# Optimization experiments

Hardware: AMD Instinct MI355X
Metric: run time of the kernel (lower is better)

The kernel has to match this reference:

```python
import jax, jax.numpy as jnp
import numpy as np

N, E, IN, HID, OUT = 100000, 1600000, 128, 128, 64


def _gcn(x, w, b, src, dst, norm, n):
    # PyG GCNConv: linear transform, then normalized scatter-add aggregation
    h = x @ w                                  # [N, F_out]
    msg = h[src] * norm[:, None]               # gather + scale, [E', F_out]
    agg = jax.ops.segment_sum(msg, dst, num_segments=n)
    return agg + b


def setup_inputs() -> dict:
    key = jax.random.key(0)
    ks = jax.random.split(key, 10)
    s = 0.05
    return {
        "X": jax.random.normal(ks[0], (N, IN), jnp.float32),
        "edge_index": jax.random.randint(ks[1], (2, E), 0, N, jnp.int64),
        "unused": 0,
        "gw1": jax.random.normal(ks[2], (IN, HID), jnp.float32) * s,
        "gb1": jnp.zeros((HID,), jnp.float32),
        "lw1": jax.random.normal(ks[3], (IN, HID), jnp.float32) * s,
        "lb1": jnp.zeros((HID,), jnp.float32),
        "gw2": jax.random.normal(ks[4], (HID, HID), jnp.float32) * s,
        "gb2": jnp.zeros((HID,), jnp.float32),
        "lw2": jax.random.normal(ks[5], (HID, HID), jnp.float32) * s,
        "lb2": jnp.zeros((HID,), jnp.float32),
        "gw3": jax.random.normal(ks[6], (HID, HID), jnp.float32) * s,
        "gb3": jnp.zeros((HID,), jnp.float32),
        "lw3": jax.random.normal(ks[7], (HID, HID), jnp.float32) * s,
        "lb3": jnp.zeros((HID,), jnp.float32),
        "fcw": jax.random.normal(ks[8], (HID, OUT), jnp.float32) * s,
        "fcb": jnp.zeros((OUT,), jnp.float32),
    }


def reference(X, edge_index, unused, gw1, gb1, lw1, lb1, gw2, gb2, lw2, lb2,
              gw3, gb3, lw3, lb3, fcw, fcb):
    n = X.shape[0]
    loop = jnp.arange(n)
    src = jnp.concatenate([edge_index[0], loop])   # self-loops appended
    dst = jnp.concatenate([edge_index[1], loop])
    deg = jax.ops.segment_sum(jnp.ones_like(dst, dtype=X.dtype), dst, num_segments=n)
    dis = jnp.where(deg > 0, jax.lax.rsqrt(jnp.maximum(deg, 1e-12)), 0.0)
    norm = dis[src] * dis[dst]                     # D^-1/2 (A+I) D^-1/2 weights

    lrelu = lambda v: jax.nn.leaky_relu(v, negative_slope=0.01)
    h = lrelu(_gcn(X, gw1, gb1, src, dst, norm, n) + X @ lw1 + lb1)
    h = lrelu(_gcn(h, gw2, gb2, src, dst, norm, n) + h @ lw2 + lb2)
    h = lrelu(_gcn(h, gw3, gb3, src, dst, norm, n) + h @ lw3 + lb3)
    y = h @ fcw + fcb
    return (h, y)
```

## Files before the change

### kernel.cpp

```cpp
#include <hip/hip_runtime.h>
#include <cstdint>
#include <cstddef>


typedef __attribute__((ext_vector_type(4))) float f32x4;
typedef __attribute__((ext_vector_type(8))) short bf16x8;
typedef unsigned short u16;

#define G_CHUNKS 256

__device__ __forceinline__ float bf2f(unsigned int u) {
  union { unsigned int i; float f; } v;
  v.i = u << 16;
  return v.f;
}
__device__ __forceinline__ u16 f2bf(float f) {
  union { float f; unsigned int i; } v;
  v.f = f;
  unsigned int i = v.i;
  return (u16)((i + 0x7FFFu + ((i >> 16) & 1u)) >> 16);
}


__global__ __launch_bounds__(256) void k_hist(const int* __restrict__ ei,
                                              int* __restrict__ ghist,
                                              int E, int B, int chunk) {
  __shared__ int h[512];
  for (int t = threadIdx.x; t < B; t += 256) h[t] = 0;
  __syncthreads();
  const int g = blockIdx.x;
  const int beg = g * chunk;
  const int end = min(beg + chunk, E);
  for (int e = beg + threadIdx.x; e < end; e += 256)
    atomicAdd(&h[ei[E + e] >> 8], 1);
  __syncthreads();
  for (int t = threadIdx.x; t < B; t += 256) ghist[(size_t)t * G_CHUNKS + g] = h[t];
}

__global__ __launch_bounds__(256) void k_hscan(int* __restrict__ ghist,
                                               int* __restrict__ btot) {
  __shared__ int sm[256];
  int* p = ghist + (size_t)blockIdx.x * G_CHUNKS;
  const int t = threadIdx.x;
  int v = p[t];
  sm[t] = v;
  __syncthreads();
  for (int off = 1; off < 256; off <<= 1) {
    int u = (t >= off) ? sm[t - off] : 0;
    __syncthreads();
    sm[t] += u;
    __syncthreads();
  }
  p[t] = sm[t] - v;
  if (t == 255) btot[blockIdx.x] = sm[255];
}

__global__ __launch_bounds__(512) void k_bscan(const int* __restrict__ btot,
                                               int* __restrict__ boff, int B,
                                               int* __restrict__ rowptr, int n,
                                               int E, int tot) {
  __shared__ int sm[512];
  const int t = threadIdx.x;
  int v = (t < B) ? btot[t] : 0;
  sm[t] = v;
  __syncthreads();
  for (int off = 1; off < 512; off <<= 1) {
    int u = (t >= off) ? sm[t - off] : 0;
    __syncthreads();
    sm[t] += u;
    __syncthreads();
  }
  if (t < B) boff[t] = sm[t] - v;
  if (t == 0) {
    boff[B] = E;
    rowptr[n] = tot;
  }
}

__global__ __launch_bounds__(256) void k_scatter(const int* __restrict__ ei,
                                                 const int* __restrict__ ghist,
                                                 const int* __restrict__ boff,
                                                 unsigned int* __restrict__ ebuf,
                                                 int E, int B, int chunk) {
  __shared__ int off[512];
  const int g = blockIdx.x;
  for (int t = threadIdx.x; t < B; t += 256)
    off[t] = boff[t] + ghist[(size_t)t * G_CHUNKS + g];
  __syncthreads();
  const int beg = g * chunk;
  const int end = min(beg + chunk, E);
  for (int e = beg + threadIdx.x; e < end; e += 256) {
    int s = ei[e];
    int d = ei[E + e];
    int pos = atomicAdd(&off[d >> 8], 1);
    ebuf[pos] = ((unsigned int)s << 8) | (unsigned int)(d & 255);
  }
}

__global__ __launch_bounds__(256) void k_cfill(const unsigned int* __restrict__ ebuf,
                                               const int* __restrict__ boff,
                                               int* __restrict__ rowptr,
                                               int* __restrict__ col,
                                               float* __restrict__ dis, int n) {
  __shared__ int cnt[256];
  __shared__ int fl[256];
  const int b = blockIdx.x;
  const int t = threadIdx.x;
  const int beg = boff[b];
  const int end = boff[b + 1];
  const int node0 = b << 8;
  const int nn = min(256, n - node0);
  cnt[t] = 0;
  __syncthreads();
  for (int e = beg + t; e < end; e += 256)
    atomicAdd(&cnt[ebuf[e] & 255u], 1);
  __syncthreads();
  int v = cnt[t];
  __shared__ int sm[256];
  sm[t] = v;
  __syncthreads();
  for (int off = 1; off < 256; off <<= 1) {
    int u = (t >= off) ? sm[t - off] : 0;
    __syncthreads();
    sm[t] += u;
    __syncthreads();
  }
  if (t < nn) {
    int excl = sm[t] - v;
    int rbase = beg + node0 + t + excl;
    int i = node0 + t;
    rowptr[i] = rbase;
    col[rbase] = i;
    fl[t] = rbase + 1;
    dis[i] = rsqrtf((float)(v + 1));
  }
  __syncthreads();
  for (int e = beg + t; e < end; e += 256) {
    unsigned int pk = ebuf[e];
    int pos = atomicAdd(&fl[pk & 255u], 1);
    col[pos] = (int)(pk >> 8);
  }
}


__global__ __launch_bounds__(256) void k_cvt(const float* __restrict__ src,
                                             const float* __restrict__ dis,
                                             u16* __restrict__ dstb,
                                             u16* __restrict__ dsts, int total8) {
  int i = blockIdx.x * 256 + threadIdx.x;
  if (i >= total8) return;
  size_t b = (size_t)i * 8;
  float ds = dis[i >> 4];
  float4 a0 = *(const float4*)(src + b);
  float4 a1 = *(const float4*)(src + b + 4);
  u16 ob[8] = {f2bf(a0.x), f2bf(a0.y), f2bf(a0.z), f2bf(a0.w),
               f2bf(a1.x), f2bf(a1.y), f2bf(a1.z), f2bf(a1.w)};
  u16 os[8] = {f2bf(a0.x * ds), f2bf(a0.y * ds), f2bf(a0.z * ds), f2bf(a0.w * ds),
               f2bf(a1.x * ds), f2bf(a1.y * ds), f2bf(a1.z * ds), f2bf(a1.w * ds)};
  *(ulonglong2*)(dstb + b) = *(ulonglong2*)ob;
  *(ulonglong2*)(dsts + b) = *(ulonglong2*)os;
}

__global__ __launch_bounds__(128) void k_prep(const float* __restrict__ w0,
                                              const float* __restrict__ w1,
                                              const float* __restrict__ w2,
                                              const float* __restrict__ w3,
                                              const float* __restrict__ w4,
                                              const float* __restrict__ w5,
                                              const float* __restrict__ g1,
                                              const float* __restrict__ l1,
                                              const float* __restrict__ g2,
                                              const float* __restrict__ l2,
                                              const float* __restrict__ g3,
                                              const float* __restrict__ l3,
                                              const float* __restrict__ fcw,
                                              u16* __restrict__ wt,
                                              float* __restrict__ bias,
                                              u16* __restrict__ fcT) {
  int bx = blockIdx.x;
  if (bx < 768) {
    int z = bx >> 7, nr = bx & 127, k = threadIdx.x;
    const float* Ws[6] = {w0, w1, w2, w3, w4, w5};
    wt[(size_t)z * 16384 + nr * 128 + k] = f2bf(Ws[z][k * 128 + nr]);
  } else if (bx < 771) {
    int t = (bx - 768) * 128 + threadIdx.x;
    if (t < 384) {
      const float* gs[3] = {g1, g2, g3};
      const float* ls[3] = {l1, l2, l3};
      bias[t] = gs[t >> 7][t & 127] + ls[t >> 7][t & 127];
    }
  } else {
    int nr = bx - 771;
    int k = threadIdx.x;
    fcT[nr * 128 + k] = f2bf(fcw[k * 64 + nr]);
  }
}

__global__ __launch_bounds__(256, 4) void k_spmv_bf(const int* __restrict__ rowptr,
                                                    const int* __restrict__ col,
                                                    const float* __restrict__ dis,
                                                    const u16* __restrict__ Xs,
                                                    u16* __restrict__ SXb, int n) {
  const int wave = threadIdx.x >> 6;
  const int lane = threadIdx.x & 63;
  const int i = blockIdx.x * 4 + wave;
  if (i >= n) return;
  int j = rowptr[i];
  const int end = rowptr[i + 1];
  float ax = 0.f, ay = 0.f;

#define ROWQ(c) (*(const unsigned int*)(Xs + (size_t)(c) * 128 + lane * 2))
#define ACC(q)  do { unsigned int _q = (q); \
                     ax += bf2f(_q & 0xffffu); ay += bf2f(_q >> 16); } while (0)

  for (; (j & 3) && j < end; ++j) ACC(ROWQ(col[j]));
  for (; j + 7 < end; j += 8) {
    int4 c0 = *(const int4*)(col + j);
    int4 c1 = *(const int4*)(col + j + 4);
    unsigned int q0 = ROWQ(c0.x), q1 = ROWQ(c0.y), q2 = ROWQ(c0.z), q3 = ROWQ(c0.w);
    unsigned int q4 = ROWQ(c1.x), q5 = ROWQ(c1.y), q6 = ROWQ(c1.z), q7 = ROWQ(c1.w);
    ACC(q0); ACC(q1); ACC(q2); ACC(q3);
    ACC(q4); ACC(q5); ACC(q6); ACC(q7);
  }
  if (j + 3 < end) {
    int4 c0 = *(const int4*)(col + j);
    unsigned int q0 = ROWQ(c0.x), q1 = ROWQ(c0.y), q2 = ROWQ(c0.z), q3 = ROWQ(c0.w);
    ACC(q0); ACC(q1); ACC(q2); ACC(q3);
    j += 4;
  }
  for (; j < end; ++j) ACC(ROWQ(col[j]));
#undef ROWQ
#undef ACC

  float di = dis[i];
  ax *= di;
  ay *= di;
  unsigned int o = (unsigned int)f2bf(ax) | ((unsigned int)f2bf(ay) << 16);
  *(unsigned int*)(SXb + (size_t)i * 128 + lane * 2) = o;
}

__global__ __launch_bounds__(256, 6) void k_mfma(const u16* __restrict__ A0,
                                                 const u16* __restrict__ A1,
                                                 const u16* __restrict__ W0T,
                                                 const u16* __restrict__ W1T,
                                                 const float* __restrict__ bias,
                                                 const float* __restrict__ dis,
                                                 u16* __restrict__ outb,
                                                 u16* __restrict__ outs,
                                                 float* __restrict__ outf, int M) {
  const int lane = threadIdx.x & 63;
  const int wv = threadIdx.x >> 6;
  const int row0 = blockIdx.x * 128 + wv * 32;
  const int c0off = blockIdx.y * 64;
  const int r = lane & 15;
  const int kg = lane >> 4;

  f32x4 acc[2][4];
#pragma unroll
  for (int a = 0; a < 2; ++a)
#pragma unroll
    for (int j = 0; j < 4; ++j) acc[a][j] = (f32x4){0.f, 0.f, 0.f, 0.f};

  const int ra0 = min(row0 + r, M - 1);
  const int ra1 = min(row0 + 16 + r, M - 1);

#pragma unroll
  for (int p = 0; p < 2; ++p) {
    const u16* A = p ? A1 : A0;
    const u16* WT = p ? W1T : W0T;
#pragma unroll
    for (int kk = 0; kk < 4; ++kk) {
      const int k0 = kk * 32 + kg * 8;
      bf16x8 a0 = *(const bf16x8*)(A + (size_t)ra0 * 128 + k0);
      bf16x8 a1 = *(const bf16x8*)(A + (size_t)ra1 * 128 + k0);
#pragma unroll
      for (int j = 0; j < 4; ++j) {
        bf16x8 b = *(const bf16x8*)(WT + (size_t)(c0off + j * 16 + r) * 128 + k0);
        acc[0][j] = __builtin_amdgcn_mfma_f32_16x16x32_bf16(a0, b, acc[0][j], 0, 0, 0);
        acc[1][j] = __builtin_amdgcn_mfma_f32_16x16x32_bf16(a1, b, acc[1][j], 0, 0, 0);
      }
    }
  }

#pragma unroll
  for (int rf = 0; rf < 2; ++rf)
#pragma unroll
    for (int e = 0; e < 4; ++e) {
      const int row = row0 + rf * 16 + kg * 4 + e;
      if (row >= M) continue;
      const float ds = outs ? dis[row] : 0.f;
#pragma unroll
      for (int j = 0; j < 4; ++j) {
        const int c = c0off + j * 16 + r;
        float v = acc[rf][j][e] + bias[c];
        v = (v > 0.f) ? v : 0.01f * v;
        if (outf) outf[(size_t)row * 128 + c] = v;
        if (outb) outb[(size_t)row * 128 + c] = f2bf(v);
        if (outs) outs[(size_t)row * 128 + c] = f2bf(v * ds);
      }
    }
}

__global__ __launch_bounds__(256) void k_fc_mfma(const u16* __restrict__ hb3,
                                                 const u16* __restrict__ fcT,
                                                 const float* __restrict__ fcb,
                                                 float* __restrict__ y, int M) {
  const int lane = threadIdx.x & 63;
  const int wv = threadIdx.x >> 6;
  const int row0 = blockIdx.x * 128 + wv * 32;
  const int r = lane & 15;
  const int kg = lane >> 4;

  f32x4 acc[2][4];
#pragma unroll
  for (int a = 0; a < 2; ++a)
#pragma unroll
    for (int j = 0; j < 4; ++j) acc[a][j] = (f32x4){0.f, 0.f, 0.f, 0.f};

  const int ra0 = min(row0 + r, M - 1);
  const int ra1 = min(row0 + 16 + r, M - 1);

#pragma unroll
  for (int kk = 0; kk < 4; ++kk) {
    const int k0 = kk * 32 + kg * 8;
    bf16x8 a0 = *(const bf16x8*)(hb3 + (size_t)ra0 * 128 + k0);
    bf16x8 a1 = *(const bf16x8*)(hb3 + (size_t)ra1 * 128 + k0);
#pragma unroll
    for (int j = 0; j < 4; ++j) {
      bf16x8 b = *(const bf16x8*)(fcT + (size_t)(j * 16 + r) * 128 + k0);
      acc[0][j] = __builtin_amdgcn_mfma_f32_16x16x32_bf16(a0, b, acc[0][j], 0, 0, 0);
      acc[1][j] = __builtin_amdgcn_mfma_f32_16x16x32_bf16(a1, b, acc[1][j], 0, 0, 0);
    }
  }

#pragma unroll
  for (int rf = 0; rf < 2; ++rf)
#pragma unroll
    for (int e = 0; e < 4; ++e) {
      const int row = row0 + rf * 16 + kg * 4 + e;
      if (row >= M) continue;
#pragma unroll
      for (int j = 0; j < 4; ++j) {
        const int c = j * 16 + r;
        y[(size_t)row * 64 + c] = acc[rf][j][e] + fcb[c];
      }
    }
}


extern "C" void kernel_launch(void* const* d_in, const int* in_sizes, int n_in,
                              void* d_out, int out_size, void* d_ws, size_t ws_size,
                              hipStream_t stream) {
  const float* X  = (const float*)d_in[0];
  const int* ei   = (const int*)d_in[1];
  const float* gw1 = (const float*)d_in[3];
  const float* gb1 = (const float*)d_in[4];
  const float* lw1 = (const float*)d_in[5];
  const float* lb1 = (const float*)d_in[6];
  const float* gw2 = (const float*)d_in[7];
  const float* gb2 = (const float*)d_in[8];
  const float* lw2 = (const float*)d_in[9];
  const float* lb2 = (const float*)d_in[10];
  const float* gw3 = (const float*)d_in[11];
  const float* gb3 = (const float*)d_in[12];
  const float* lw3 = (const float*)d_in[13];
  const float* lb3 = (const float*)d_in[14];
  const float* fcw = (const float*)d_in[15];
  const float* fcb = (const float*)d_in[16];

  const int n = in_sizes[0] / 128;
  const int E = in_sizes[1] / 2;
  const int tot = E + n;
  const int B = (n + 255) >> 8;
  const int chunk = (E + G_CHUNKS - 1) / G_CHUNKS;

  char* ws = (char*)d_ws;
  size_t off = 0;
  auto alloc = [&](size_t bytes) -> void* {
    void* p = ws + off;
    off = (off + bytes + 255) & ~(size_t)255;
    return p;
  };
  int* ghist   = (int*)alloc((size_t)B * G_CHUNKS * 4);
  int* btot    = (int*)alloc(512 * 4);
  int* boff    = (int*)alloc((size_t)(B + 1) * 4);
  int* rowptr  = (int*)alloc((size_t)(n + 1) * 4);
  float* dis   = (float*)alloc((size_t)n * 4);
  int* col     = (int*)alloc((size_t)tot * 4);
  unsigned int* ebuf = (unsigned int*)alloc((size_t)E * 4);
  u16* Xb      = (u16*)alloc((size_t)n * 128 * 2);
  u16* Xs      = (u16*)alloc((size_t)n * 128 * 2);
  u16* SXb     = (u16*)alloc((size_t)n * 128 * 2);
  u16* WT      = (u16*)alloc((size_t)6 * 16384 * 2);
  u16* fcT     = (u16*)alloc((size_t)64 * 128 * 2);
  float* bias  = (float*)alloc(384 * 4);

  float* outh = (float*)d_out;
  float* outy = outh + (size_t)n * 128;
  u16* hb = (u16*)outy;

  const int gM = (n + 127) / 128;
  const int gW = (n + 3) / 4;
  const int g8 = (n * 128 / 8 + 255) / 256;

  k_hist<<<G_CHUNKS, 256, 0, stream>>>(ei, ghist, E, B, chunk);
  k_hscan<<<B, 256, 0, stream>>>(ghist, btot);
  k_bscan<<<1, 512, 0, stream>>>(btot, boff, B, rowptr, n, E, tot);
  k_scatter<<<G_CHUNKS, 256, 0, stream>>>(ei, ghist, boff, ebuf, E, B, chunk);
  k_cfill<<<B, 256, 0, stream>>>(ebuf, boff, rowptr, col, dis, n);

  k_cvt<<<g8, 256, 0, stream>>>(X, dis, Xb, Xs, n * 128 / 8);
  k_prep<<<835, 128, 0, stream>>>(gw1, lw1, gw2, lw2, gw3, lw3,
                                  gb1, lb1, gb2, lb2, gb3, lb3, fcw,
                                  WT, bias, fcT);

  k_spmv_bf<<<gW, 256, 0, stream>>>(rowptr, col, dis, Xs, SXb, n);
  k_mfma<<<dim3(gM, 2), 256, 0, stream>>>(SXb, Xb, WT, WT + 16384, bias, dis,
                                          hb, Xs, nullptr, n);
  k_spmv_bf<<<gW, 256, 0, stream>>>(rowptr, col, dis, Xs, SXb, n);
  k_mfma<<<dim3(gM, 2), 256, 0, stream>>>(SXb, hb, WT + 2 * 16384, WT + 3 * 16384,
                                          bias + 128, dis, Xb, Xs, nullptr, n);
  k_spmv_bf<<<gW, 256, 0, stream>>>(rowptr, col, dis, Xs, SXb, n);
  k_mfma<<<dim3(gM, 2), 256, 0, stream>>>(SXb, Xb, WT + 4 * 16384, WT + 5 * 16384,
                                          bias + 256, dis, hb, nullptr, outh, n);
  k_fc_mfma<<<gM, 256, 0, stream>>>(hb, fcT, fcb, outy, n);
}
```

Measured before the change: 470.8 us.

## Use half-wave per row in SpMV and narrow MFMA column tiles

The SpMV kernel now gives each 128-wide row to a 32-lane half-wave, and each lane loads 8-byte bf16 chunks instead of 4-byte ones. Each block therefore covers 8 rows and more gathers are in flight per wave. The fused GEMM kernel now computes 32 output columns per block instead of 64 across a 4-wide grid, with occupancy hints raised to 8. The GEMM split doubles how often the A operand is read, in exchange for fewer registers and more blocks.

```diff
diff --git a/kernel.cpp b/kernel.cpp
--- a/kernel.cpp
+++ b/kernel.cpp
@@ -196,35 +196,37 @@
   }
 }
 
-__global__ __launch_bounds__(256, 4) void k_spmv_bf(const int* __restrict__ rowptr,
+__global__ __launch_bounds__(256, 8) void k_spmv_bf(const int* __restrict__ rowptr,
                                                     const int* __restrict__ col,
                                                     const float* __restrict__ dis,
                                                     const u16* __restrict__ Xs,
                                                     u16* __restrict__ SXb, int n) {
-  const int wave = threadIdx.x >> 6;
-  const int lane = threadIdx.x & 63;
-  const int i = blockIdx.x * 4 + wave;
+  const int tid = threadIdx.x;
+  const int half = (tid >> 5) & 1;
+  const int sub = tid & 31;
+  const int i = blockIdx.x * 8 + (tid >> 6) * 2 + half;
   if (i >= n) return;
   int j = rowptr[i];
   const int end = rowptr[i + 1];
-  float ax = 0.f, ay = 0.f;
-
-#define ROWQ(c) (*(const unsigned int*)(Xs + (size_t)(c) * 128 + lane * 2))
-#define ACC(q)  do { unsigned int _q = (q); \
-                     ax += bf2f(_q & 0xffffu); ay += bf2f(_q >> 16); } while (0)
+  float a0 = 0.f, a1 = 0.f, a2 = 0.f, a3 = 0.f;
+
+#define ROWQ(c) (*(const uint2*)(Xs + (size_t)(c) * 128 + sub * 4))
+#define ACC(q)  do { uint2 _q = (q); \
+                     a0 += bf2f(_q.x & 0xffffu); a1 += bf2f(_q.x >> 16); \
+                     a2 += bf2f(_q.y & 0xffffu); a3 += bf2f(_q.y >> 16); } while (0)
 
   for (; (j & 3) && j < end; ++j) ACC(ROWQ(col[j]));
   for (; j + 7 < end; j += 8) {
     int4 c0 = *(const int4*)(col + j);
     int4 c1 = *(const int4*)(col + j + 4);
-    unsigned int q0 = ROWQ(c0.x), q1 = ROWQ(c0.y), q2 = ROWQ(c0.z), q3 = ROWQ(c0.w);
-    unsigned int q4 = ROWQ(c1.x), q5 = ROWQ(c1.y), q6 = ROWQ(c1.z), q7 = ROWQ(c1.w);
+    uint2 q0 = ROWQ(c0.x), q1 = ROWQ(c0.y), q2 = ROWQ(c0.z), q3 = ROWQ(c0.w);
+    uint2 q4 = ROWQ(c1.x), q5 = ROWQ(c1.y), q6 = ROWQ(c1.z), q7 = ROWQ(c1.w);
     ACC(q0); ACC(q1); ACC(q2); ACC(q3);
     ACC(q4); ACC(q5); ACC(q6); ACC(q7);
   }
   if (j + 3 < end) {
     int4 c0 = *(const int4*)(col + j);
-    unsigned int q0 = ROWQ(c0.x), q1 = ROWQ(c0.y), q2 = ROWQ(c0.z), q3 = ROWQ(c0.w);
+    uint2 q0 = ROWQ(c0.x), q1 = ROWQ(c0.y), q2 = ROWQ(c0.z), q3 = ROWQ(c0.w);
     ACC(q0); ACC(q1); ACC(q2); ACC(q3);
     j += 4;
   }
@@ -232,14 +234,14 @@
 #undef ROWQ
 #undef ACC
 
-  float di = dis[i];
-  ax *= di;
-  ay *= di;
-  unsigned int o = (unsigned int)f2bf(ax) | ((unsigned int)f2bf(ay) << 16);
-  *(unsigned int*)(SXb + (size_t)i * 128 + lane * 2) = o;
-}
-
-__global__ __launch_bounds__(256, 6) void k_mfma(const u16* __restrict__ A0,
+  const float di = dis[i];
+  uint2 o;
+  o.x = (unsigned int)f2bf(a0 * di) | ((unsigned int)f2bf(a1 * di) << 16);
+  o.y = (unsigned int)f2bf(a2 * di) | ((unsigned int)f2bf(a3 * di) << 16);
+  *(uint2*)(SXb + (size_t)i * 128 + sub * 4) = o;
+}
+
+__global__ __launch_bounds__(256, 8) void k_mfma(const u16* __restrict__ A0,
                                                  const u16* __restrict__ A1,
                                                  const u16* __restrict__ W0T,
                                                  const u16* __restrict__ W1T,
@@ -251,15 +253,15 @@
   const int lane = threadIdx.x & 63;
   const int wv = threadIdx.x >> 6;
   const int row0 = blockIdx.x * 128 + wv * 32;
-  const int c0off = blockIdx.y * 64;
+  const int c0off = blockIdx.y * 32;
   const int r = lane & 15;
   const int kg = lane >> 4;
 
-  f32x4 acc[2][4];
+  f32x4 acc[2][2];
 #pragma unroll
   for (int a = 0; a < 2; ++a)
 #pragma unroll
-    for (int j = 0; j < 4; ++j) acc[a][j] = (f32x4){0.f, 0.f, 0.f, 0.f};
+    for (int j = 0; j < 2; ++j) acc[a][j] = (f32x4){0.f, 0.f, 0.f, 0.f};
 
   const int ra0 = min(row0 + r, M - 1);
   const int ra1 = min(row0 + 16 + r, M - 1);
@@ -274,7 +276,7 @@
       bf16x8 a0 = *(const bf16x8*)(A + (size_t)ra0 * 128 + k0);
       bf16x8 a1 = *(const bf16x8*)(A + (size_t)ra1 * 128 + k0);
 #pragma unroll
-      for (int j = 0; j < 4; ++j) {
+      for (int j = 0; j < 2; ++j) {
         bf16x8 b = *(const bf16x8*)(WT + (size_t)(c0off + j * 16 + r) * 128 + k0);
         acc[0][j] = __builtin_amdgcn_mfma_f32_16x16x32_bf16(a0, b, acc[0][j], 0, 0, 0);
         acc[1][j] = __builtin_amdgcn_mfma_f32_16x16x32_bf16(a1, b, acc[1][j], 0, 0, 0);
@@ -290,7 +292,7 @@
       if (row >= M) continue;
       const float ds = outs ? dis[row] : 0.f;
 #pragma unroll
-      for (int j = 0; j < 4; ++j) {
+      for (int j = 0; j < 2; ++j) {
         const int c = c0off + j * 16 + r;
         float v = acc[rf][j][e] + bias[c];
         v = (v > 0.f) ? v : 0.01f * v;
@@ -400,7 +402,7 @@
   u16* hb = (u16*)outy;
 
   const int gM = (n + 127) / 128;
-  const int gW = (n + 3) / 4;
+  const int gW = (n + 7) / 8;
   const int g8 = (n * 128 / 8 + 255) / 256;
 
   k_hist<<<G_CHUNKS, 256, 0, stream>>>(ei, ghist, E, B, chunk);
@@ -415,13 +417,13 @@
                                   WT, bias, fcT);
 
   k_spmv_bf<<<gW, 256, 0, stream>>>(rowptr, col, dis, Xs, SXb, n);
-  k_mfma<<<dim3(gM, 2), 256, 0, stream>>>(SXb, Xb, WT, WT + 16384, bias, dis,
+  k_mfma<<<dim3(gM, 4), 256, 0, stream>>>(SXb, Xb, WT, WT + 16384, bias, dis,
                                           hb, Xs, nullptr, n);
   k_spmv_bf<<<gW, 256, 0, stream>>>(rowptr, col, dis, Xs, SXb, n);
-  k_mfma<<<dim3(gM, 2), 256, 0, stream>>>(SXb, hb, WT + 2 * 16384, WT + 3 * 16384,
+  k_mfma<<<dim3(gM, 4), 256, 0, stream>>>(SXb, hb, WT + 2 * 16384, WT + 3 * 16384,
                                           bias + 128, dis, Xb, Xs, nullptr, n);
   k_spmv_bf<<<gW, 256, 0, stream>>>(rowptr, col, dis, Xs, SXb, n);
-  k_mfma<<<dim3(gM, 2), 256, 0, stream>>>(SXb, Xb, WT + 4 * 16384, WT + 5 * 16384,
+  k_mfma<<<dim3(gM, 4), 256, 0, stream>>>(SXb, Xb, WT + 4 * 16384, WT + 5 * 16384,
                                           bias + 256, dis, hb, nullptr, outh, n);
   k_fc_mfma<<<gM, 256, 0, stream>>>(hb, fcT, fcb, outy, n);
 }
```

New measurement: 443.0 us. 1.06x faster.
